# Performance work log

Measured on AMD Instinct MI355X. Metric: run time of the kernel, lower is better.

Reference implementation:

```python
import jax, jax.numpy as jnp
import numpy as np

NUM_CLASSES = 256
FEATURE_DIM = 768
BATCH = 128
SIM_BALANCE = 0.7
TIER1 = 50.0
TIER2 = 10.0
TOPK = 5


def _l2norm(x):
    return x / jnp.linalg.norm(x, axis=1, keepdims=True)


def build_edge_weights(class_features, context_features, w1, b1, w2, b2,
                       co_occurrence, instance_counts):
    """Vectorized, faithful translation of VisualFeatureGraph.build_graph."""
    N = class_features.shape[0]
    dt = class_features.dtype
    co = co_occurrence.astype(dt)            # [N,N], diag is 0
    cnt = instance_counts.astype(dt)         # [N]

    vs = _l2norm(class_features) @ _l2norm(class_features).T    # visual_sim [N,N]
    cs = _l2norm(context_features) @ _l2norm(context_features).T  # context_sim
    combined = SIM_BALANCE * vs + (1.0 - SIM_BALANCE) * cs

    # ---- Tier 1: co > TIER1 ----
    # sim_proj(f_i - f_j): exploit linearity of first layer: (f_i-f_j)@W1 = a_i - a_j
    a = class_features @ w1                                    # [N, D/2]
    h = jax.nn.relu(a[:, None, :] - a[None, :, :] + b1)        # [N,N,D/2]
    sim_weight = jax.nn.sigmoid(h @ w2 + b2)[..., 0]           # [N,N]
    ratio = (jnp.minimum(cnt[:, None], cnt[None, :]) /
             jnp.maximum(jnp.maximum(cnt[:, None], cnt[None, :]), 1.0))
    e1 = combined * sim_weight * ratio

    # ---- Tier 2: TIER2 < co <= TIER1 ----
    # shared neighbors k: co[i,k]>T1 and co[j,k]>T1 (k=i,j auto-excluded: diag=0
    # and co[i,j]<=T1 for tier-2 pairs)
    A = (co > TIER1).astype(dt)                                # [N,N]
    M = vs * A
    shared_sum = M @ M.T                                       # sum_k vs[i,k]*vs[j,k]
    shared_cnt = A @ A.T
    avg_sim = shared_sum / jnp.maximum(shared_cnt, 1.0)
    conf = co / TIER1
    e2 = jnp.where(shared_cnt > 0,
                   conf * combined + (1.0 - conf) * avg_sim,
                   conf * combined)

    # ---- Tier 3: co <= TIER2 ----
    # top-5 neighbors per row by co-occurrence among co > TIER2 (diag=0 and
    # co[i,j]<=TIER2 for tier-3 pairs, so i and j are auto-excluded)
    top_vals, top_idx = jax.lax.top_k(co, TOPK)                # [N,K]
    valid = top_vals > TIER2                                   # [N,K]
    ii = top_idx[:, None, :, None]                             # [N,1,K,1]
    jj = top_idx[None, :, None, :]                             # [1,N,1,K]
    co_cross = co[ii, jj]                                      # co[i_neigh, j_neigh] [N,N,K,K]
    vs_cross = vs[ii, jj]
    vs_in = jnp.take_along_axis(vs, top_idx, axis=1)           # vs[i, i_neigh] [N,K]
    mask = valid[:, None, :, None] & valid[None, :, None, :] & (co_cross > 0)
    w = (top_vals[:, None, :, None] * top_vals[None, :, None, :]) / TIER1
    w = jnp.where(mask, w, 0.0)
    sim = vs_in[:, None, :, None] * vs_in[None, :, None, :] * vs_cross
    trans = jnp.sum(w * sim, axis=(2, 3))                      # [N,N]
    tot = jnp.sum(w, axis=(2, 3))
    e3 = jnp.where(tot > 0, trans / jnp.where(tot > 0, tot, 1.0), 0.1 * cs)

    tier1_mask = co > TIER1
    tier2_mask = (co > TIER2) & ~tier1_mask
    E = jnp.where(tier1_mask, e1, jnp.where(tier2_mask, e2, e3))
    E = E * (1.0 - jnp.eye(N, dtype=dt))                       # i==j skipped
    mx = jnp.max(E)
    E = jnp.where(mx > 0, E / jnp.where(mx > 0, mx, 1.0), E)
    return E


def setup_inputs() -> dict:
    key = jax.random.key(0)
    ks = jax.random.split(key, 8)
    N, D, B = NUM_CLASSES, FEATURE_DIM, BATCH
    x = jax.random.normal(ks[0], (B, N, D), dtype=jnp.float32)
    class_features = jax.random.normal(ks[1], (N, D), dtype=jnp.float32) * 0.05
    context_features = jax.random.normal(ks[2], (N, D), dtype=jnp.float32) * 0.05
    w1 = jax.random.normal(ks[3], (D, D // 2), dtype=jnp.float32) * (1.0 / np.sqrt(D))
    b1 = jnp.zeros((D // 2,), dtype=jnp.float32)
    w2 = jax.random.normal(ks[4], (D // 2, 1), dtype=jnp.float32) * (1.0 / np.sqrt(D // 2))
    b2 = jnp.zeros((1,), dtype=jnp.float32)
    co = jax.random.randint(ks[5], (N, N), 0, 121, dtype=jnp.int32)
    co = (co + co.T) // 2                                      # symmetric like update_features
    co = co * (1 - jnp.eye(N, dtype=jnp.int32))                # zero diagonal
    instance_counts = jax.random.randint(ks[6], (N,), 1, 1001, dtype=jnp.int32)
    return {"x": x, "class_features": class_features,
            "context_features": context_features,
            "w1": w1, "b1": b1, "w2": w2, "b2": b2,
            "co_occurrence": co, "instance_counts": instance_counts}


def reference(x, class_features, context_features, w1, b1, w2, b2,
              co_occurrence, instance_counts):
    E = build_edge_weights(class_features, context_features, w1, b1, w2, b2,
                           co_occurrence, instance_counts)
    # torch.bmm(E.expand(B,-1,-1), x) == einsum over shared node dim
    return x + jnp.einsum('ij,bjd->bid', E, x)
```

## Files before the change

### kernel.cpp

```cpp
#include <hip/hip_runtime.h>
#include <hip/hip_bf16.h>
#include <math.h>

#define N 256
#define D 768
#define BATCH 128

typedef float f32x4 __attribute__((ext_vector_type(4)));
typedef short bf16x8 __attribute__((ext_vector_type(8)));

static __device__ __forceinline__ unsigned short f2bf(float f) {
    unsigned int u = __float_as_uint(f);
    u += 0x7fffu + ((u >> 16) & 1u);
    return (unsigned short)(u >> 16);
}
static __device__ __forceinline__ unsigned int pack2bf(float lo, float hi) {
    unsigned int a = __float_as_uint(lo);
    unsigned int b = __float_as_uint(hi);
    a += 0x7fffu + ((a >> 16) & 1u);
    b += 0x7fffu + ((b >> 16) & 1u);
    return (a >> 16) | (b & 0xffff0000u);
}

__global__ void k_norm(const float* __restrict__ cf, const float* __restrict__ ctx,
                       float* __restrict__ vsn, float* __restrict__ csn) {
    int row = blockIdx.x;
    const float* src;
    float* dst;
    if (row < N) { src = cf  + row * D;       dst = vsn + row * D; }
    else         { src = ctx + (row - N) * D; dst = csn + (row - N) * D; }
    int t = threadIdx.x;
    float s = 0.f;
    for (int d = t; d < D; d += 256) { float v = src[d]; s += v * v; }
    __shared__ float red[256];
    red[t] = s; __syncthreads();
    for (int off = 128; off > 0; off >>= 1) {
        if (t < off) red[t] += red[t + off];
        __syncthreads();
    }
    float inv = 1.0f / sqrtf(red[0]);
    for (int d = t; d < D; d += 256) dst[d] = src[d] * inv;
}

__global__ void k_a2(const float* __restrict__ cf, const float* __restrict__ w1,
                     float* __restrict__ a) {
    int bi = blockIdx.x;
    int i0 = (bi / 12) * 32, j0 = (bi % 12) * 32;
    __shared__ float Ci[64][33], Wj[64][33];
    int t = threadIdx.x;
    int tx = t & 15, ty = t >> 4;
    float a00 = 0.f, a01 = 0.f, a10 = 0.f, a11 = 0.f;
    for (int k0 = 0; k0 < 768; k0 += 64) {
        #pragma unroll
        for (int s = 0; s < 8; s++) {
            int idx = s * 256 + t;
            int row = idx >> 6, kc = idx & 63;
            Ci[kc][row] = cf[(i0 + row) * 768 + k0 + kc];
            int kr = idx >> 5, col = idx & 31;
            Wj[kr][col] = w1[(k0 + kr) * 384 + j0 + col];
        }
        __syncthreads();
        #pragma unroll 4
        for (int kk = 0; kk < 64; kk++) {
            float iv0 = Ci[kk][ty * 2], iv1 = Ci[kk][ty * 2 + 1];
            float jv0 = Wj[kk][tx * 2], jv1 = Wj[kk][tx * 2 + 1];
            a00 += iv0 * jv0; a01 += iv0 * jv1;
            a10 += iv1 * jv0; a11 += iv1 * jv1;
        }
        __syncthreads();
    }
    a[(i0 + ty * 2)     * 384 + j0 + tx * 2]     = a00;
    a[(i0 + ty * 2)     * 384 + j0 + tx * 2 + 1] = a01;
    a[(i0 + ty * 2 + 1) * 384 + j0 + tx * 2]     = a10;
    a[(i0 + ty * 2 + 1) * 384 + j0 + tx * 2 + 1] = a11;
}

__global__ void k_gram2(const float* __restrict__ vsn, const float* __restrict__ csn,
                        float* __restrict__ vs, float* __restrict__ cs) {
    int bx = blockIdx.x;
    const float* S = (bx >= 64) ? csn : vsn;
    float* O       = (bx >= 64) ? cs  : vs;
    int bi = bx & 63;
    int i0 = (bi >> 3) * 32, j0 = (bi & 7) * 32;
    __shared__ float Li[64][33], Lj[64][33];
    int t = threadIdx.x;
    int tx = t & 15, ty = t >> 4;
    float a00 = 0.f, a01 = 0.f, a10 = 0.f, a11 = 0.f;
    for (int k0 = 0; k0 < 768; k0 += 64) {
        #pragma unroll
        for (int s = 0; s < 8; s++) {
            int idx = s * 256 + t;
            int row = idx >> 6, kc = idx & 63;
            Li[kc][row] = S[(i0 + row) * 768 + k0 + kc];
            Lj[kc][row] = S[(j0 + row) * 768 + k0 + kc];
        }
        __syncthreads();
        #pragma unroll 4
        for (int kk = 0; kk < 64; kk++) {
            float iv0 = Li[kk][ty * 2], iv1 = Li[kk][ty * 2 + 1];
            float jv0 = Lj[kk][tx * 2], jv1 = Lj[kk][tx * 2 + 1];
            a00 += iv0 * jv0; a01 += iv0 * jv1;
            a10 += iv1 * jv0; a11 += iv1 * jv1;
        }
        __syncthreads();
    }
    O[(i0 + ty * 2)     * 256 + j0 + tx * 2]     = a00;
    O[(i0 + ty * 2)     * 256 + j0 + tx * 2 + 1] = a01;
    O[(i0 + ty * 2 + 1) * 256 + j0 + tx * 2]     = a10;
    O[(i0 + ty * 2 + 1) * 256 + j0 + tx * 2 + 1] = a11;
}

__global__ __launch_bounds__(256) void k_e1t(
    const float* __restrict__ a, const float* __restrict__ b1,
    const float* __restrict__ w2, const float* __restrict__ b2,
    const float* __restrict__ vs, const float* __restrict__ cs,
    const int* __restrict__ ic, float* __restrict__ e1) {
    int i0 = (blockIdx.x >> 4) * 16, j0 = (blockIdx.x & 15) * 16;
    __shared__ float ai[16][388], ajm[16][388];
    __shared__ float sw2[384];
    int t = threadIdx.x;
    for (int idx = t; idx < 16 * 96; idx += 256) {
        int r = idx / 96, c = (idx % 96) * 4;
        *(float4*)&ai[r][c] = *(const float4*)(a + (i0 + r) * 384 + c);
        float4 u  = *(const float4*)(a + (j0 + r) * 384 + c);
        float4 bb = *(const float4*)(b1 + c);
        u.x -= bb.x; u.y -= bb.y; u.z -= bb.z; u.w -= bb.w;
        *(float4*)&ajm[r][c] = u;
    }
    for (int k = t; k < 384; k += 256) sw2[k] = w2[k];
    __syncthreads();
    int tx = t & 15, ty = t >> 4;
    float s = 0.f;
    #pragma unroll 4
    for (int k4 = 0; k4 < 96; k4++) {
        float4 xv = *(const float4*)&ai[ty][k4 * 4];
        float4 yv = *(const float4*)&ajm[tx][k4 * 4];
        float4 wv = *(const float4*)&sw2[k4 * 4];
        s += fmaxf(xv.x - yv.x, 0.f) * wv.x;
        s += fmaxf(xv.y - yv.y, 0.f) * wv.y;
        s += fmaxf(xv.z - yv.z, 0.f) * wv.z;
        s += fmaxf(xv.w - yv.w, 0.f) * wv.w;
    }
    int i = i0 + ty, j = j0 + tx;
    float sig = 1.0f / (1.0f + expf(-(s + b2[0])));
    float comb = 0.7f * vs[i * 256 + j] + 0.3f * cs[i * 256 + j];
    float ci = (float)ic[i], cj = (float)ic[j];
    float mn = fminf(ci, cj), mx = fmaxf(ci, cj);
    float ratio = mn / fmaxf(mx, 1.0f);
    e1[i * 256 + j] = comb * sig * ratio;
}

__global__ void k_shared2(const int* __restrict__ co, const float* __restrict__ vs,
                          float* __restrict__ ss, float* __restrict__ sc) {
    int bi = blockIdx.x;
    int i0 = (bi >> 3) * 32, j0 = (bi & 7) * 32;
    __shared__ float Mi[64][33], Ai[64][33], Mj[64][33], Aj[64][33];
    int t = threadIdx.x;
    int tx = t & 15, ty = t >> 4;
    float s00=0.f,s01=0.f,s10=0.f,s11=0.f;
    float c00=0.f,c01=0.f,c10=0.f,c11=0.f;
    for (int k0 = 0; k0 < 256; k0 += 64) {
        #pragma unroll
        for (int s = 0; s < 8; s++) {
            int idx = s * 256 + t;
            int row = idx >> 6, kc = idx & 63;
            int ci = co[(i0 + row) * 256 + k0 + kc];
            float aa = ci > 50 ? 1.f : 0.f;
            Ai[kc][row] = aa;
            Mi[kc][row] = aa * vs[(i0 + row) * 256 + k0 + kc];
            int cj = co[(j0 + row) * 256 + k0 + kc];
            float ab = cj > 50 ? 1.f : 0.f;
            Aj[kc][row] = ab;
            Mj[kc][row] = ab * vs[(j0 + row) * 256 + k0 + kc];
        }
        __syncthreads();
        #pragma unroll 4
        for (int kk = 0; kk < 64; kk++) {
            float mi0 = Mi[kk][ty*2], mi1 = Mi[kk][ty*2+1];
            float ai0 = Ai[kk][ty*2], ai1 = Ai[kk][ty*2+1];
            float mj0 = Mj[kk][tx*2], mj1 = Mj[kk][tx*2+1];
            float aj0 = Aj[kk][tx*2], aj1 = Aj[kk][tx*2+1];
            s00 += mi0*mj0; s01 += mi0*mj1; s10 += mi1*mj0; s11 += mi1*mj1;
            c00 += ai0*aj0; c01 += ai0*aj1; c10 += ai1*aj0; c11 += ai1*aj1;
        }
        __syncthreads();
    }
    ss[(i0+ty*2)  *256 + j0+tx*2]   = s00; ss[(i0+ty*2)  *256 + j0+tx*2+1] = s01;
    ss[(i0+ty*2+1)*256 + j0+tx*2]   = s10; ss[(i0+ty*2+1)*256 + j0+tx*2+1] = s11;
    sc[(i0+ty*2)  *256 + j0+tx*2]   = c00; sc[(i0+ty*2)  *256 + j0+tx*2+1] = c01;
    sc[(i0+ty*2+1)*256 + j0+tx*2]   = c10; sc[(i0+ty*2+1)*256 + j0+tx*2+1] = c11;
}

__global__ void k_topk2(const int* __restrict__ co, float* __restrict__ topv,
                        int* __restrict__ topi) {
    int t = threadIdx.x;
    int lane = t & 63;
    int row = blockIdx.x * 4 + (t >> 6);
    int4 v4 = *(const int4*)(co + row * 256 + lane * 4);
    int key[4];
    key[0] = v4.x * 256 + (255 - (lane * 4 + 0));
    key[1] = v4.y * 256 + (255 - (lane * 4 + 1));
    key[2] = v4.z * 256 + (255 - (lane * 4 + 2));
    key[3] = v4.w * 256 + (255 - (lane * 4 + 3));
    for (int r = 0; r < 5; r++) {
        int best = key[0];
        #pragma unroll
        for (int e = 1; e < 4; e++) best = max(best, key[e]);
        #pragma unroll
        for (int off = 32; off > 0; off >>= 1) best = max(best, __shfl_xor(best, off, 64));
        int kidx = 255 - (best & 255);
        int val = best >> 8;
        if (lane == 0) { topv[row * 5 + r] = (float)val; topi[row * 5 + r] = kidx; }
        if ((kidx >> 2) == lane) key[kidx & 3] = -1;
    }
}

__global__ void k_assemble(const int* __restrict__ co, const float* __restrict__ vs,
                           const float* __restrict__ cs, const float* __restrict__ e1,
                           const float* __restrict__ ss, const float* __restrict__ sc,
                           const float* __restrict__ topv, const int* __restrict__ topi,
                           float* __restrict__ E, float* __restrict__ partials) {
    int i = blockIdx.x, j = threadIdx.x;
    int cij = co[i * 256 + j];
    float e;
    if (i == j) {
        e = 0.f;
    } else if (cij > 50) {
        e = e1[i * 256 + j];
    } else if (cij > 10) {
        float conf = (float)cij / 50.0f;
        float comb = 0.7f * vs[i * 256 + j] + 0.3f * cs[i * 256 + j];
        float cnt = sc[i * 256 + j];
        float avg = ss[i * 256 + j] / fmaxf(cnt, 1.f);
        e = (cnt > 0.f) ? conf * comb + (1.f - conf) * avg : conf * comb;
    } else {
        float tvi[5], tvj[5]; int tii[5], tij[5];
        #pragma unroll
        for (int k = 0; k < 5; k++) {
            tvi[k] = topv[i * 5 + k]; tii[k] = topi[i * 5 + k];
            tvj[k] = topv[j * 5 + k]; tij[k] = topi[j * 5 + k];
        }
        float trans = 0.f, tot = 0.f;
        #pragma unroll
        for (int k = 0; k < 5; k++) {
            if (!(tvi[k] > 10.f)) continue;
            float vin_i = vs[i * 256 + tii[k]];
            #pragma unroll
            for (int l = 0; l < 5; l++) {
                if (!(tvj[l] > 10.f)) continue;
                int cc = co[tii[k] * 256 + tij[l]];
                if (cc <= 0) continue;
                float w = tvi[k] * tvj[l] / 50.f;
                float sim = vin_i * vs[j * 256 + tij[l]] * vs[tii[k] * 256 + tij[l]];
                trans += w * sim; tot += w;
            }
        }
        e = (tot > 0.f) ? trans / tot : 0.1f * cs[i * 256 + j];
    }
    E[i * 256 + j] = e;
    __shared__ float red[256];
    red[j] = e; __syncthreads();
    for (int off = 128; off > 0; off >>= 1) {
        if (j < off) red[j] = fmaxf(red[j], red[j + off]);
        __syncthreads();
    }
    if (j == 0) partials[i] = red[0];
}

__global__ void k_ep(const float* __restrict__ E, const float* __restrict__ partials,
                     unsigned short* __restrict__ Ep) {
    __shared__ float red[256];
    int t = threadIdx.x;
    red[t] = partials[t]; __syncthreads();
    for (int off = 128; off > 0; off >>= 1) {
        if (t < off) red[t] = fmaxf(red[t], red[t + off]);
        __syncthreads();
    }
    float mx = red[0];
    float s = (mx > 0.f) ? 1.0f / mx : 1.0f;
    int base = (blockIdx.x * 256 + t) * 4;
    float4 e4 = *(const float4*)(E + base);
    float ev[4] = {e4.x, e4.y, e4.z, e4.w};
    unsigned short o[4];
    #pragma unroll
    for (int q = 0; q < 4; q++) {
        int g = base + q;
        float v = s * ev[q] + (((g >> 8) == (g & 255)) ? 1.0f : 0.0f);
        o[q] = f2bf(v);
    }
    uint2 w;
    w.x = (unsigned int)o[0] | ((unsigned int)o[1] << 16);
    w.y = (unsigned int)o[2] | ((unsigned int)o[3] << 16);
    *(uint2*)(Ep + base) = w;
}

#define PEP 264
#define PXT 40
__global__ __launch_bounds__(256, 1) void k_einsum_mfma(
    const unsigned short* __restrict__ Ep, const float* __restrict__ x,
    float* __restrict__ out) {
    extern __shared__ unsigned short smem[];
    unsigned short* eplds = smem;
    unsigned short* xt    = smem + 256 * PEP;
    int t = threadIdx.x;
    int b = blockIdx.y;
    int d0 = blockIdx.x * 128;

    #pragma unroll
    for (int it = 0; it < 32; it++) {
        int c = it * 256 + t;
        uint4 v = *(const uint4*)(Ep + (size_t)c * 8);
        *(uint4*)&eplds[(c >> 5) * PEP + (c & 31) * 8] = v;
    }

    int dcol = t & 127;
    int kp = (t >> 7) * 2;
    const float* xb = x + ((size_t)b * 256) * 768 + d0 + dcol;

    int lane = t & 63;
    int lq = lane >> 4, l15 = lane & 15;
    int i0w = (t >> 6) * 64;

    f32x4 acc[4][8];
    #pragma unroll
    for (int gm = 0; gm < 4; gm++)
        #pragma unroll
        for (int gn = 0; gn < 8; gn++)
            #pragma unroll
            for (int e = 0; e < 4; e++) acc[gm][gn][e] = 0.f;

    float r0[8], r1[8];
    #pragma unroll
    for (int s = 0; s < 8; s++) {
        int k = kp + 4 * s;
        r0[s] = xb[k * 768];
        r1[s] = xb[(k + 1) * 768];
    }

    for (int kt = 0; kt < 8; kt++) {
        #pragma unroll
        for (int s = 0; s < 8; s++) {
            int k = kp + 4 * s;
            *(unsigned int*)&xt[dcol * PXT + k] = pack2bf(r0[s], r1[s]);
        }
        __syncthreads();
        if (kt < 7) {
            const float* xn = xb + (kt + 1) * 32 * 768;
            #pragma unroll
            for (int s = 0; s < 8; s++) {
                int k = kp + 4 * s;
                r0[s] = xn[k * 768];
                r1[s] = xn[(k + 1) * 768];
            }
        }
        int kg = kt * 32 + lq * 8;
        bf16x8 av[4], bv[8];
        #pragma unroll
        for (int g = 0; g < 4; g++)
            av[g] = *(const bf16x8*)&eplds[(i0w + g * 16 + l15) * PEP + kg];
        #pragma unroll
        for (int g = 0; g < 8; g++)
            bv[g] = *(const bf16x8*)&xt[(g * 16 + l15) * PXT + lq * 8];
        #pragma unroll
        for (int gm = 0; gm < 4; gm++)
            #pragma unroll
            for (int gn = 0; gn < 8; gn++)
                acc[gm][gn] = __builtin_amdgcn_mfma_f32_16x16x32_bf16(
                    av[gm], bv[gn], acc[gm][gn], 0, 0, 0);
        __syncthreads();
    }

    float* ob = out + ((size_t)b * 256) * 768 + d0;
    #pragma unroll
    for (int gm = 0; gm < 4; gm++) {
        #pragma unroll
        for (int gn = 0; gn < 8; gn++) {
            #pragma unroll
            for (int r = 0; r < 4; r++) {
                int i = i0w + gm * 16 + lq * 4 + r;
                int d = gn * 16 + l15;
                ob[(size_t)i * 768 + d] = acc[gm][gn][r];
            }
        }
    }
}

extern "C" void kernel_launch(void* const* d_in, const int* in_sizes, int n_in,
                              void* d_out, int out_size, void* d_ws, size_t ws_size,
                              hipStream_t stream) {
    const float* x   = (const float*)d_in[0];
    const float* cf  = (const float*)d_in[1];
    const float* ctx = (const float*)d_in[2];
    const float* w1  = (const float*)d_in[3];
    const float* b1  = (const float*)d_in[4];
    const float* w2  = (const float*)d_in[5];
    const float* b2  = (const float*)d_in[6];
    const int*   co  = (const int*)d_in[7];
    const int*   ic  = (const int*)d_in[8];
    float* out = (float*)d_out;

    float* ws   = (float*)d_ws;
    float* vsn  = ws;
    float* csn  = vsn + 196608;
    float* a    = csn + 196608;
    float* vs   = a + 98304;
    float* cs   = vs + 65536;
    float* e1   = cs + 65536;
    float* ss   = e1 + 65536;
    float* sc   = ss + 65536;
    float* E    = sc + 65536;
    float* topv = E + 65536;
    int*   topi = (int*)(topv + 1280);
    float* partials = (float*)(topi + 1280);
    unsigned short* Ep = (unsigned short*)(partials + 256);

    k_norm<<<512, 256, 0, stream>>>(cf, ctx, vsn, csn);
    k_a2<<<96, 256, 0, stream>>>(cf, w1, a);
    k_gram2<<<128, 256, 0, stream>>>(vsn, csn, vs, cs);
    k_e1t<<<256, 256, 0, stream>>>(a, b1, w2, b2, vs, cs, ic, e1);
    k_shared2<<<64, 256, 0, stream>>>(co, vs, ss, sc);
    k_topk2<<<64, 256, 0, stream>>>(co, topv, topi);
    k_assemble<<<256, 256, 0, stream>>>(co, vs, cs, e1, ss, sc, topv, topi, E, partials);
    k_ep<<<64, 256, 0, stream>>>(E, partials, Ep);
    size_t lds_bytes = (size_t)(256 * PEP + 128 * PXT) * sizeof(unsigned short);
    k_einsum_mfma<<<dim3(6, BATCH), 256, lds_bytes, stream>>>(Ep, x, out);
}
```

Measured before the change: 287.5 us.

## Merge independent prep kernels and rewrite einsum with transposed LDS reads

Independent preprocessing kernels (norm, a-projection, top-k, then e1 and shared-neighbor grams) are merged into two launches that dispatch by block index, cutting launch overhead and serialization. The final einsum kernel no longer stages the whole bf16 edge matrix in LDS. It streams E fragments directly from global into registers and double-buffers a small bf16 x tile that is read with ds_read_b64_tr_b16. This lowers LDS use so two blocks can fit per CU, and output is written with float4 stores. The cost is hand-written inline asm and more register pressure.

```diff
diff --git a/kernel.cpp b/kernel.cpp
--- a/kernel.cpp
+++ b/kernel.cpp
@@ -22,57 +22,81 @@
     return (a >> 16) | (b & 0xffff0000u);
 }
 
-__global__ void k_norm(const float* __restrict__ cf, const float* __restrict__ ctx,
-                       float* __restrict__ vsn, float* __restrict__ csn) {
-    int row = blockIdx.x;
-    const float* src;
-    float* dst;
-    if (row < N) { src = cf  + row * D;       dst = vsn + row * D; }
-    else         { src = ctx + (row - N) * D; dst = csn + (row - N) * D; }
+__global__ void k_stage1(const float* __restrict__ cf, const float* __restrict__ ctx,
+                         float* __restrict__ vsn, float* __restrict__ csn,
+                         const float* __restrict__ w1, float* __restrict__ a,
+                         const int* __restrict__ co, float* __restrict__ topv,
+                         int* __restrict__ topi) {
+    __shared__ float sm[2 * 64 * 33];
+    int bx = blockIdx.x;
     int t = threadIdx.x;
-    float s = 0.f;
-    for (int d = t; d < D; d += 256) { float v = src[d]; s += v * v; }
-    __shared__ float red[256];
-    red[t] = s; __syncthreads();
-    for (int off = 128; off > 0; off >>= 1) {
-        if (t < off) red[t] += red[t + off];
-        __syncthreads();
-    }
-    float inv = 1.0f / sqrtf(red[0]);
-    for (int d = t; d < D; d += 256) dst[d] = src[d] * inv;
-}
-
-__global__ void k_a2(const float* __restrict__ cf, const float* __restrict__ w1,
-                     float* __restrict__ a) {
-    int bi = blockIdx.x;
-    int i0 = (bi / 12) * 32, j0 = (bi % 12) * 32;
-    __shared__ float Ci[64][33], Wj[64][33];
-    int t = threadIdx.x;
-    int tx = t & 15, ty = t >> 4;
-    float a00 = 0.f, a01 = 0.f, a10 = 0.f, a11 = 0.f;
-    for (int k0 = 0; k0 < 768; k0 += 64) {
-        #pragma unroll
-        for (int s = 0; s < 8; s++) {
-            int idx = s * 256 + t;
-            int row = idx >> 6, kc = idx & 63;
-            Ci[kc][row] = cf[(i0 + row) * 768 + k0 + kc];
-            int kr = idx >> 5, col = idx & 31;
-            Wj[kr][col] = w1[(k0 + kr) * 384 + j0 + col];
-        }
-        __syncthreads();
-        #pragma unroll 4
-        for (int kk = 0; kk < 64; kk++) {
-            float iv0 = Ci[kk][ty * 2], iv1 = Ci[kk][ty * 2 + 1];
-            float jv0 = Wj[kk][tx * 2], jv1 = Wj[kk][tx * 2 + 1];
-            a00 += iv0 * jv0; a01 += iv0 * jv1;
-            a10 += iv1 * jv0; a11 += iv1 * jv1;
-        }
-        __syncthreads();
-    }
-    a[(i0 + ty * 2)     * 384 + j0 + tx * 2]     = a00;
-    a[(i0 + ty * 2)     * 384 + j0 + tx * 2 + 1] = a01;
-    a[(i0 + ty * 2 + 1) * 384 + j0 + tx * 2]     = a10;
-    a[(i0 + ty * 2 + 1) * 384 + j0 + tx * 2 + 1] = a11;
+    if (bx < 512) {
+        int row = bx;
+        const float* src;
+        float* dst;
+        if (row < N) { src = cf  + row * D;       dst = vsn + row * D; }
+        else         { src = ctx + (row - N) * D; dst = csn + (row - N) * D; }
+        float s = 0.f;
+        for (int d = t; d < D; d += 256) { float v = src[d]; s += v * v; }
+        float* red = sm;
+        red[t] = s; __syncthreads();
+        for (int off = 128; off > 0; off >>= 1) {
+            if (t < off) red[t] += red[t + off];
+            __syncthreads();
+        }
+        float inv = 1.0f / sqrtf(red[0]);
+        for (int d = t; d < D; d += 256) dst[d] = src[d] * inv;
+    } else if (bx < 608) {
+        int bi = bx - 512;
+        int i0 = (bi / 12) * 32, j0 = (bi % 12) * 32;
+        float (*Ci)[33] = (float(*)[33])sm;
+        float (*Wj)[33] = (float(*)[33])(sm + 64 * 33);
+        int tx = t & 15, ty = t >> 4;
+        float a00 = 0.f, a01 = 0.f, a10 = 0.f, a11 = 0.f;
+        for (int k0 = 0; k0 < 768; k0 += 64) {
+            #pragma unroll
+            for (int s = 0; s < 8; s++) {
+                int idx = s * 256 + t;
+                int row = idx >> 6, kc = idx & 63;
+                Ci[kc][row] = cf[(i0 + row) * 768 + k0 + kc];
+                int kr = idx >> 5, col = idx & 31;
+                Wj[kr][col] = w1[(k0 + kr) * 384 + j0 + col];
+            }
+            __syncthreads();
+            #pragma unroll 4
+            for (int kk = 0; kk < 64; kk++) {
+                float iv0 = Ci[kk][ty * 2], iv1 = Ci[kk][ty * 2 + 1];
+                float jv0 = Wj[kk][tx * 2], jv1 = Wj[kk][tx * 2 + 1];
+                a00 += iv0 * jv0; a01 += iv0 * jv1;
+                a10 += iv1 * jv0; a11 += iv1 * jv1;
+            }
+            __syncthreads();
+        }
+        a[(i0 + ty * 2)     * 384 + j0 + tx * 2]     = a00;
+        a[(i0 + ty * 2)     * 384 + j0 + tx * 2 + 1] = a01;
+        a[(i0 + ty * 2 + 1) * 384 + j0 + tx * 2]     = a10;
+        a[(i0 + ty * 2 + 1) * 384 + j0 + tx * 2 + 1] = a11;
+    } else {
+        int lane = t & 63;
+        int row = (bx - 608) * 4 + (t >> 6);
+        int4 v4 = *(const int4*)(co + row * 256 + lane * 4);
+        int key[4];
+        key[0] = v4.x * 256 + (255 - (lane * 4 + 0));
+        key[1] = v4.y * 256 + (255 - (lane * 4 + 1));
+        key[2] = v4.z * 256 + (255 - (lane * 4 + 2));
+        key[3] = v4.w * 256 + (255 - (lane * 4 + 3));
+        for (int r = 0; r < 5; r++) {
+            int best = key[0];
+            #pragma unroll
+            for (int e = 1; e < 4; e++) best = max(best, key[e]);
+            #pragma unroll
+            for (int off = 32; off > 0; off >>= 1) best = max(best, __shfl_xor(best, off, 64));
+            int kidx = 255 - (best & 255);
+            int val = best >> 8;
+            if (lane == 0) { topv[row * 5 + r] = (float)val; topi[row * 5 + r] = kidx; }
+            if ((kidx >> 2) == lane) key[kidx & 3] = -1;
+        }
+    }
 }
 
 __global__ void k_gram2(const float* __restrict__ vsn, const float* __restrict__ csn,
@@ -110,108 +134,89 @@
     O[(i0 + ty * 2 + 1) * 256 + j0 + tx * 2 + 1] = a11;
 }
 
-__global__ __launch_bounds__(256) void k_e1t(
-    const float* __restrict__ a, const float* __restrict__ b1,
-    const float* __restrict__ w2, const float* __restrict__ b2,
-    const float* __restrict__ vs, const float* __restrict__ cs,
-    const int* __restrict__ ic, float* __restrict__ e1) {
-    int i0 = (blockIdx.x >> 4) * 16, j0 = (blockIdx.x & 15) * 16;
-    __shared__ float ai[16][388], ajm[16][388];
-    __shared__ float sw2[384];
+__global__ void k_stage3(const float* __restrict__ a, const float* __restrict__ b1,
+                         const float* __restrict__ w2, const float* __restrict__ b2,
+                         const float* __restrict__ vs, const float* __restrict__ cs,
+                         const int* __restrict__ ic, float* __restrict__ e1,
+                         const int* __restrict__ co, float* __restrict__ ss,
+                         float* __restrict__ sc) {
+    __shared__ float sm[12800];
+    int bx = blockIdx.x;
     int t = threadIdx.x;
-    for (int idx = t; idx < 16 * 96; idx += 256) {
-        int r = idx / 96, c = (idx % 96) * 4;
-        *(float4*)&ai[r][c] = *(const float4*)(a + (i0 + r) * 384 + c);
-        float4 u  = *(const float4*)(a + (j0 + r) * 384 + c);
-        float4 bb = *(const float4*)(b1 + c);
-        u.x -= bb.x; u.y -= bb.y; u.z -= bb.z; u.w -= bb.w;
-        *(float4*)&ajm[r][c] = u;
-    }
-    for (int k = t; k < 384; k += 256) sw2[k] = w2[k];
-    __syncthreads();
-    int tx = t & 15, ty = t >> 4;
-    float s = 0.f;
-    #pragma unroll 4
-    for (int k4 = 0; k4 < 96; k4++) {
-        float4 xv = *(const float4*)&ai[ty][k4 * 4];
-        float4 yv = *(const float4*)&ajm[tx][k4 * 4];
-        float4 wv = *(const float4*)&sw2[k4 * 4];
-        s += fmaxf(xv.x - yv.x, 0.f) * wv.x;
-        s += fmaxf(xv.y - yv.y, 0.f) * wv.y;
-        s += fmaxf(xv.z - yv.z, 0.f) * wv.z;
-        s += fmaxf(xv.w - yv.w, 0.f) * wv.w;
-    }
-    int i = i0 + ty, j = j0 + tx;
-    float sig = 1.0f / (1.0f + expf(-(s + b2[0])));
-    float comb = 0.7f * vs[i * 256 + j] + 0.3f * cs[i * 256 + j];
-    float ci = (float)ic[i], cj = (float)ic[j];
-    float mn = fminf(ci, cj), mx = fmaxf(ci, cj);
-    float ratio = mn / fmaxf(mx, 1.0f);
-    e1[i * 256 + j] = comb * sig * ratio;
-}
-
-__global__ void k_shared2(const int* __restrict__ co, const float* __restrict__ vs,
-                          float* __restrict__ ss, float* __restrict__ sc) {
-    int bi = blockIdx.x;
-    int i0 = (bi >> 3) * 32, j0 = (bi & 7) * 32;
-    __shared__ float Mi[64][33], Ai[64][33], Mj[64][33], Aj[64][33];
-    int t = threadIdx.x;
-    int tx = t & 15, ty = t >> 4;
-    float s00=0.f,s01=0.f,s10=0.f,s11=0.f;
-    float c00=0.f,c01=0.f,c10=0.f,c11=0.f;
-    for (int k0 = 0; k0 < 256; k0 += 64) {
-        #pragma unroll
-        for (int s = 0; s < 8; s++) {
-            int idx = s * 256 + t;
-            int row = idx >> 6, kc = idx & 63;
-            int ci = co[(i0 + row) * 256 + k0 + kc];
-            float aa = ci > 50 ? 1.f : 0.f;
-            Ai[kc][row] = aa;
-            Mi[kc][row] = aa * vs[(i0 + row) * 256 + k0 + kc];
-            int cj = co[(j0 + row) * 256 + k0 + kc];
-            float ab = cj > 50 ? 1.f : 0.f;
-            Aj[kc][row] = ab;
-            Mj[kc][row] = ab * vs[(j0 + row) * 256 + k0 + kc];
-        }
+    if (bx < 256) {
+        int i0 = (bx >> 4) * 16, j0 = (bx & 15) * 16;
+        float (*ai)[388]  = (float(*)[388])sm;
+        float (*ajm)[388] = (float(*)[388])(sm + 16 * 388);
+        float* sw2 = sm + 2 * 16 * 388;
+        for (int idx = t; idx < 16 * 96; idx += 256) {
+            int r = idx / 96, c = (idx % 96) * 4;
+            *(float4*)&ai[r][c] = *(const float4*)(a + (i0 + r) * 384 + c);
+            float4 u  = *(const float4*)(a + (j0 + r) * 384 + c);
+            float4 bb = *(const float4*)(b1 + c);
+            u.x -= bb.x; u.y -= bb.y; u.z -= bb.z; u.w -= bb.w;
+            *(float4*)&ajm[r][c] = u;
+        }
+        for (int k = t; k < 384; k += 256) sw2[k] = w2[k];
         __syncthreads();
+        int tx = t & 15, ty = t >> 4;
+        float s = 0.f;
         #pragma unroll 4
-        for (int kk = 0; kk < 64; kk++) {
-            float mi0 = Mi[kk][ty*2], mi1 = Mi[kk][ty*2+1];
-            float ai0 = Ai[kk][ty*2], ai1 = Ai[kk][ty*2+1];
-            float mj0 = Mj[kk][tx*2], mj1 = Mj[kk][tx*2+1];
-            float aj0 = Aj[kk][tx*2], aj1 = Aj[kk][tx*2+1];
-            s00 += mi0*mj0; s01 += mi0*mj1; s10 += mi1*mj0; s11 += mi1*mj1;
-            c00 += ai0*aj0; c01 += ai0*aj1; c10 += ai1*aj0; c11 += ai1*aj1;
-        }
-        __syncthreads();
-    }
-    ss[(i0+ty*2)  *256 + j0+tx*2]   = s00; ss[(i0+ty*2)  *256 + j0+tx*2+1] = s01;
-    ss[(i0+ty*2+1)*256 + j0+tx*2]   = s10; ss[(i0+ty*2+1)*256 + j0+tx*2+1] = s11;
-    sc[(i0+ty*2)  *256 + j0+tx*2]   = c00; sc[(i0+ty*2)  *256 + j0+tx*2+1] = c01;
-    sc[(i0+ty*2+1)*256 + j0+tx*2]   = c10; sc[(i0+ty*2+1)*256 + j0+tx*2+1] = c11;
-}
-
-__global__ void k_topk2(const int* __restrict__ co, float* __restrict__ topv,
-                        int* __restrict__ topi) {
-    int t = threadIdx.x;
-    int lane = t & 63;
-    int row = blockIdx.x * 4 + (t >> 6);
-    int4 v4 = *(const int4*)(co + row * 256 + lane * 4);
-    int key[4];
-    key[0] = v4.x * 256 + (255 - (lane * 4 + 0));
-    key[1] = v4.y * 256 + (255 - (lane * 4 + 1));
-    key[2] = v4.z * 256 + (255 - (lane * 4 + 2));
-    key[3] = v4.w * 256 + (255 - (lane * 4 + 3));
-    for (int r = 0; r < 5; r++) {
-        int best = key[0];
-        #pragma unroll
-        for (int e = 1; e < 4; e++) best = max(best, key[e]);
-        #pragma unroll
-        for (int off = 32; off > 0; off >>= 1) best = max(best, __shfl_xor(best, off, 64));
-        int kidx = 255 - (best & 255);
-        int val = best >> 8;
-        if (lane == 0) { topv[row * 5 + r] = (float)val; topi[row * 5 + r] = kidx; }
-        if ((kidx >> 2) == lane) key[kidx & 3] = -1;
+        for (int k4 = 0; k4 < 96; k4++) {
+            float4 xv = *(const float4*)&ai[ty][k4 * 4];
+            float4 yv = *(const float4*)&ajm[tx][k4 * 4];
+            float4 wv = *(const float4*)&sw2[k4 * 4];
+            s += fmaxf(xv.x - yv.x, 0.f) * wv.x;
+            s += fmaxf(xv.y - yv.y, 0.f) * wv.y;
+            s += fmaxf(xv.z - yv.z, 0.f) * wv.z;
+            s += fmaxf(xv.w - yv.w, 0.f) * wv.w;
+        }
+        int i = i0 + ty, j = j0 + tx;
+        float sig = 1.0f / (1.0f + expf(-(s + b2[0])));
+        float comb = 0.7f * vs[i * 256 + j] + 0.3f * cs[i * 256 + j];
+        float ci = (float)ic[i], cj = (float)ic[j];
+        float mn = fminf(ci, cj), mx = fmaxf(ci, cj);
+        float ratio = mn / fmaxf(mx, 1.0f);
+        e1[i * 256 + j] = comb * sig * ratio;
+    } else {
+        int bi = bx - 256;
+        int i0 = (bi >> 3) * 32, j0 = (bi & 7) * 32;
+        float (*Mi)[33] = (float(*)[33])sm;
+        float (*Ai)[33] = (float(*)[33])(sm + 2112);
+        float (*Mj)[33] = (float(*)[33])(sm + 4224);
+        float (*Aj)[33] = (float(*)[33])(sm + 6336);
+        int tx = t & 15, ty = t >> 4;
+        float s00=0.f,s01=0.f,s10=0.f,s11=0.f;
+        float c00=0.f,c01=0.f,c10=0.f,c11=0.f;
+        for (int k0 = 0; k0 < 256; k0 += 64) {
+            #pragma unroll
+            for (int s = 0; s < 8; s++) {
+                int idx = s * 256 + t;
+                int row = idx >> 6, kc = idx & 63;
+                int civ = co[(i0 + row) * 256 + k0 + kc];
+                float aa = civ > 50 ? 1.f : 0.f;
+                Ai[kc][row] = aa;
+                Mi[kc][row] = aa * vs[(i0 + row) * 256 + k0 + kc];
+                int cjv = co[(j0 + row) * 256 + k0 + kc];
+                float ab = cjv > 50 ? 1.f : 0.f;
+                Aj[kc][row] = ab;
+                Mj[kc][row] = ab * vs[(j0 + row) * 256 + k0 + kc];
+            }
+            __syncthreads();
+            #pragma unroll 4
+            for (int kk = 0; kk < 64; kk++) {
+                float mi0 = Mi[kk][ty*2], mi1 = Mi[kk][ty*2+1];
+                float ai0 = Ai[kk][ty*2], ai1 = Ai[kk][ty*2+1];
+                float mj0 = Mj[kk][tx*2], mj1 = Mj[kk][tx*2+1];
+                float aj0 = Aj[kk][tx*2], aj1 = Aj[kk][tx*2+1];
+                s00 += mi0*mj0; s01 += mi0*mj1; s10 += mi1*mj0; s11 += mi1*mj1;
+                c00 += ai0*aj0; c01 += ai0*aj1; c10 += ai1*aj0; c11 += ai1*aj1;
+            }
+            __syncthreads();
+        }
+        ss[(i0+ty*2)  *256 + j0+tx*2]   = s00; ss[(i0+ty*2)  *256 + j0+tx*2+1] = s01;
+        ss[(i0+ty*2+1)*256 + j0+tx*2]   = s10; ss[(i0+ty*2+1)*256 + j0+tx*2+1] = s11;
+        sc[(i0+ty*2)  *256 + j0+tx*2]   = c00; sc[(i0+ty*2)  *256 + j0+tx*2+1] = c01;
+        sc[(i0+ty*2+1)*256 + j0+tx*2]   = c10; sc[(i0+ty*2+1)*256 + j0+tx*2+1] = c11;
     }
 }
 
@@ -294,93 +299,94 @@
     *(uint2*)(Ep + base) = w;
 }
 
-#define PEP 264
-#define PXT 40
-__global__ __launch_bounds__(256, 1) void k_einsum_mfma(
+#define EINS_BUFB 9472
+
+#define EIN_BODY(KT, BB, bvC, bvN)                                              \
+  {                                                                             \
+    _Pragma("unroll")                                                           \
+    for (int s = 0; s < 4; s++) {                                               \
+      uint2 pv;                                                                 \
+      pv.x = pack2bf(xr[s].x, xr[s].y);                                         \
+      pv.y = pack2bf(xr[s].z, xr[s].w);                                         \
+      *(uint2*)((char*)xs + (BB) + wbyte + s * 32) = pv;                        \
+    }                                                                           \
+    __syncthreads();                                                            \
+    if ((KT) < 7) {                                                             \
+      const float* xn = xb + (size_t)((KT) + 1) * 32 * 768;                     \
+      _Pragma("unroll")                                                         \
+      for (int s = 0; s < 4; s++)                                               \
+        xr[s] = *(const float4*)(xn + (size_t)(jb + s) * 768);                  \
+      _Pragma("unroll")                                                         \
+      for (int nf = 0; nf < 4; nf++)                                            \
+        bvN[nf] = *(const uint4*)(eprow + (nf << 12) + ((KT) + 1) * 32);        \
+    }                                                                           \
+    uint2 a0[8], a1[8];                                                         \
+    _Pragma("unroll")                                                           \
+    for (int g = 0; g < 8; g++) {                                               \
+      unsigned ag = ra + (BB) + g * 1184;                                       \
+      asm volatile("ds_read_b64_tr_b16 %0, %1" : "=v"(a0[g]) : "v"(ag));        \
+      asm volatile("ds_read_b64_tr_b16 %0, %1 offset:144" : "=v"(a1[g]) : "v"(ag)); \
+    }                                                                           \
+    asm volatile("s_waitcnt lgkmcnt(0)" ::: "memory");                          \
+    __builtin_amdgcn_sched_barrier(0);                                          \
+    _Pragma("unroll")                                                           \
+    for (int mf = 0; mf < 8; mf++) {                                            \
+      union { uint2 u[2]; bf16x8 v; } af;                                       \
+      af.u[0] = a0[mf]; af.u[1] = a1[mf];                                       \
+      _Pragma("unroll")                                                         \
+      for (int nf = 0; nf < 4; nf++)                                            \
+        acc[mf][nf] = __builtin_amdgcn_mfma_f32_16x16x32_bf16(                  \
+            af.v, *(const bf16x8*)&bvC[nf], acc[mf][nf], 0, 0, 0);              \
+    }                                                                           \
+  }
+
+__global__ __launch_bounds__(256, 2) void k_einsum_tr(
     const unsigned short* __restrict__ Ep, const float* __restrict__ x,
     float* __restrict__ out) {
-    extern __shared__ unsigned short smem[];
-    unsigned short* eplds = smem;
-    unsigned short* xt    = smem + 256 * PEP;
+    extern __shared__ unsigned short xs[];
     int t = threadIdx.x;
     int b = blockIdx.y;
     int d0 = blockIdx.x * 128;
-
-    #pragma unroll
-    for (int it = 0; it < 32; it++) {
-        int c = it * 256 + t;
-        uint4 v = *(const uint4*)(Ep + (size_t)c * 8);
-        *(uint4*)&eplds[(c >> 5) * PEP + (c & 31) * 8] = v;
-    }
-
-    int dcol = t & 127;
-    int kp = (t >> 7) * 2;
-    const float* xb = x + ((size_t)b * 256) * 768 + d0 + dcol;
-
-    int lane = t & 63;
-    int lq = lane >> 4, l15 = lane & 15;
-    int i0w = (t >> 6) * 64;
-
-    f32x4 acc[4][8];
-    #pragma unroll
-    for (int gm = 0; gm < 4; gm++)
+    int lane = t & 63, w = t >> 6;
+    int l15 = lane & 15, lq = lane >> 4;
+
+    int dq = t & 31;
+    int jb = (t >> 5) * 4;
+    const float* xb = x + ((size_t)b * 256) * 768 + d0 + 4 * dq;
+    unsigned wbyte = (unsigned)(((dq >> 2) * 592 + (jb >> 2) * 72 + (dq & 3) * 4) * 2);
+    unsigned ra = (unsigned)(lq * 288 + l15 * 8);
+
+    const unsigned short* eprow = Ep + (((w * 64 + l15) << 8) + lq * 8);
+
+    f32x4 acc[8][4];
+    #pragma unroll
+    for (int mf = 0; mf < 8; mf++)
         #pragma unroll
-        for (int gn = 0; gn < 8; gn++)
-            #pragma unroll
-            for (int e = 0; e < 4; e++) acc[gm][gn][e] = 0.f;
-
-    float r0[8], r1[8];
-    #pragma unroll
-    for (int s = 0; s < 8; s++) {
-        int k = kp + 4 * s;
-        r0[s] = xb[k * 768];
-        r1[s] = xb[(k + 1) * 768];
-    }
-
-    for (int kt = 0; kt < 8; kt++) {
+        for (int nf = 0; nf < 4; nf++)
+            #pragma unroll
+            for (int e = 0; e < 4; e++) acc[mf][nf][e] = 0.f;
+
+    float4 xr[4];
+    #pragma unroll
+    for (int s = 0; s < 4; s++) xr[s] = *(const float4*)(xb + (size_t)(jb + s) * 768);
+    uint4 bv0[4], bv1[4];
+    #pragma unroll
+    for (int nf = 0; nf < 4; nf++) bv0[nf] = *(const uint4*)(eprow + (nf << 12));
+
+    #pragma unroll
+    for (int k2 = 0; k2 < 4; k2++) {
+        EIN_BODY(2 * k2,     0,         bv0, bv1)
+        EIN_BODY(2 * k2 + 1, EINS_BUFB, bv1, bv0)
+    }
+
+    float* ob = out + ((size_t)b * 256) * 768 + d0;
+    #pragma unroll
+    for (int mf = 0; mf < 8; mf++) {
         #pragma unroll
-        for (int s = 0; s < 8; s++) {
-            int k = kp + 4 * s;
-            *(unsigned int*)&xt[dcol * PXT + k] = pack2bf(r0[s], r1[s]);
-        }
-        __syncthreads();
-        if (kt < 7) {
-            const float* xn = xb + (kt + 1) * 32 * 768;
-            #pragma unroll
-            for (int s = 0; s < 8; s++) {
-                int k = kp + 4 * s;
-                r0[s] = xn[k * 768];
-                r1[s] = xn[(k + 1) * 768];
-            }
-        }
-        int kg = kt * 32 + lq * 8;
-        bf16x8 av[4], bv[8];
-        #pragma unroll
-        for (int g = 0; g < 4; g++)
-            av[g] = *(const bf16x8*)&eplds[(i0w + g * 16 + l15) * PEP + kg];
-        #pragma unroll
-        for (int g = 0; g < 8; g++)
-            bv[g] = *(const bf16x8*)&xt[(g * 16 + l15) * PXT + lq * 8];
-        #pragma unroll
-        for (int gm = 0; gm < 4; gm++)
-            #pragma unroll
-            for (int gn = 0; gn < 8; gn++)
-                acc[gm][gn] = __builtin_amdgcn_mfma_f32_16x16x32_bf16(
-                    av[gm], bv[gn], acc[gm][gn], 0, 0, 0);
-        __syncthreads();
-    }
-
-    float* ob = out + ((size_t)b * 256) * 768 + d0;
-    #pragma unroll
-    for (int gm = 0; gm < 4; gm++) {
-        #pragma unroll
-        for (int gn = 0; gn < 8; gn++) {
-            #pragma unroll
-            for (int r = 0; r < 4; r++) {
-                int i = i0w + gm * 16 + lq * 4 + r;
-                int d = gn * 16 + l15;
-                ob[(size_t)i * 768 + d] = acc[gm][gn][r];
-            }
+        for (int nf = 0; nf < 4; nf++) {
+            int i = w * 64 + nf * 16 + l15;
+            int d = mf * 16 + lq * 4;
+            *(float4*)(ob + (size_t)i * 768 + d) = *(float4*)&acc[mf][nf];
         }
     }
 }
@@ -414,14 +420,10 @@
     float* partials = (float*)(topi + 1280);
     unsigned short* Ep = (unsigned short*)(partials + 256);
 
-    k_norm<<<512, 256, 0, stream>>>(cf, ctx, vsn, csn);
-    k_a2<<<96, 256, 0, stream>>>(cf, w1, a);
+    k_stage1<<<672, 256, 0, stream>>>(cf, ctx, vsn, csn, w1, a, co, topv, topi);
     k_gram2<<<128, 256, 0, stream>>>(vsn, csn, vs, cs);
-    k_e1t<<<256, 256, 0, stream>>>(a, b1, w2, b2, vs, cs, ic, e1);
-    k_shared2<<<64, 256, 0, stream>>>(co, vs, ss, sc);
-    k_topk2<<<64, 256, 0, stream>>>(co, topv, topi);
+    k_stage3<<<320, 256, 0, stream>>>(a, b1, w2, b2, vs, cs, ic, e1, co, ss, sc);
     k_assemble<<<256, 256, 0, stream>>>(co, vs, cs, e1, ss, sc, topv, topi, E, partials);
     k_ep<<<64, 256, 0, stream>>>(E, partials, Ep);
-    size_t lds_bytes = (size_t)(256 * PEP + 128 * PXT) * sizeof(unsigned short);
-    k_einsum_mfma<<<dim3(6, BATCH), 256, lds_bytes, stream>>>(Ep, x, out);
-}
+    k_einsum_tr<<<dim3(6, BATCH), 256, 2 * EINS_BUFB, stream>>>(Ep, x, out);
+}
```

Measured after the change: 290.3 us. No clear change (+1.0%).
